# Kernel optimization log

Hardware: AMD Instinct MI355X
Metric: run time of the kernel (lower is better)

Reference implementation:

```python
import jax, jax.numpy as jnp
import numpy as np

BETA = 0.25
TEMP = 1.0
K = 1024          # codebook_size
DIM = 256         # dim == z_dim


def setup_inputs() -> dict:
    key = jax.random.key(0)
    k1, k2, k3 = jax.random.split(key, 3)
    x = jax.random.normal(k1, (8, 4096, DIM), dtype=jnp.float32)
    # Linear: kaiming_uniform -> sqrt(3/fan_in) * U(-1,1); bias init_bias=0 -> zeros
    W = np.sqrt(3.0 / DIM) * (jax.random.uniform(k2, (DIM, DIM), dtype=jnp.float32) * 2 - 1)
    b = jnp.zeros((DIM,), dtype=jnp.float32)
    # embedding: uniform(-1/K, 1/K)
    emb = jax.random.uniform(k3, (K, DIM), dtype=jnp.float32,
                             minval=-1.0 / K, maxval=1.0 / K)
    return {"x": x, "W": W, "b": b, "emb": emb}


def reference(x, W, b, emb):
    # proj_in: x @ W.T + b
    z = jnp.einsum('bld,od->blo', x, W) + b                     # [B, L, D]
    # squared-L2 distances to codebook (use_norm=False branch)
    dist = (jnp.sum(z * z, axis=-1, keepdims=True)
            + jnp.sum(emb * emb, axis=1)
            - 2.0 * jnp.einsum('bld,nd->bln', z, emb))           # [B, L, K]
    indices = jnp.argmin(dist, axis=-1)                          # [B, L] int
    # ste_prob computed in torch forward (affects grads via one_hot, not outputs)
    quant = emb[indices]                                         # [B, L, D]
    # commitment + codebook loss (training=True)
    loss = (BETA * jnp.mean((jax.lax.stop_gradient(quant) - z) ** 2)
            + jnp.mean((quant - jax.lax.stop_gradient(z)) ** 2))
    # straight-through estimator
    quant = z + jax.lax.stop_gradient(quant - z)
    return quant, indices, loss
```

## Files before the change

kernel.cpp:

```cpp
#include <hip/hip_runtime.h>
#include <hip/hip_bf16.h>

#define TT 32768
#define DD 256
#define KK 1024
#define B_S 5e-4f

typedef __attribute__((ext_vector_type(8)))  short bf16x8;
typedef __attribute__((ext_vector_type(4)))  short bf16x4s;
typedef __attribute__((ext_vector_type(16))) float f32x16;

static inline __device__ short f2bf(float v) {
    __hip_bfloat16 h = __float2bfloat16(v);
    return __builtin_bit_cast(short, h);
}
static inline __device__ float bf2f(short s) {
    __hip_bfloat16 h = __builtin_bit_cast(__hip_bfloat16, s);
    return __bfloat162float(h);
}

static inline __device__ void gload16(const void* g, void* l) {
    __builtin_amdgcn_global_load_lds(
        (const __attribute__((address_space(1))) void*)g,
        (__attribute__((address_space(3))) void*)l,
        16, 0, 0);
}

__global__ void k_ee(const float* __restrict__ emb, float* __restrict__ ee,
                     int* __restrict__ g_nf) {
    if (blockIdx.x == 0 && threadIdx.x == 0) g_nf[0] = 0;
    int n = blockIdx.x * 256 + threadIdx.x;
    if (n >= KK) return;
    const float4* r = (const float4*)(emb + (size_t)n * DD);
    float s = 0.f;
#pragma unroll
    for (int i = 0; i < DD / 4; ++i) {
        float4 v = r[i];
        s += v.x * v.x + v.y * v.y + v.z * v.z + v.w * v.w;
    }
    ee[n] = s;
}

__global__ void k_pack(const float* __restrict__ emb, short* __restrict__ pemb,
                       float4* __restrict__ embP4) {
    int u = blockIdx.x * 256 + threadIdx.x;
    int lane = u & 63;
    int ks  = (u >> 6) & 1, nb = (u >> 7) & 3;
    int kbi = (u >> 9) & 7, nc = (u >> 12) & 7;
    int n = nc * 128 + nb * 32 + (lane & 31);
    int k = kbi * 32 + ks * 16 + (lane >> 5) * 8;
    const float* src = emb + (size_t)n * DD + k;
    float4 v0 = *(const float4*)(src);
    float4 v1 = *(const float4*)(src + 4);
    bf16x8 hb = { f2bf(v0.x), f2bf(v0.y), f2bf(v0.z), f2bf(v0.w),
                  f2bf(v1.x), f2bf(v1.y), f2bf(v1.z), f2bf(v1.w) };
    *(bf16x8*)(pemb + (size_t)u * 8) = hb;
    embP4[(size_t)(k >> 2) * KK + n]       = v0;
    embP4[(size_t)((k >> 2) + 1) * KK + n] = v1;
}

#define PW 40

__launch_bounds__(256, 2)
__global__ void k_proj(const float* __restrict__ x, const float* __restrict__ W,
                       const float* __restrict__ bias, float* __restrict__ z) {
    __shared__ __align__(16) short Ax[3][64 * PW];
    __shared__ __align__(16) short Bw[3][256 * PW];
    const int tid = threadIdx.x;
    const int w = tid >> 6, lane = tid & 63;
    const int l31 = lane & 31, h = lane >> 5;
    const int t0 = blockIdx.x * 64;
    const int wt = (w & 1) * 32;
    const int wc = (w >> 1) * 128;

    f32x16 acc[4];
#pragma unroll
    for (int cb = 0; cb < 4; ++cb)
#pragma unroll
        for (int r = 0; r < 16; ++r) acc[cb][r] = 0.f;

    for (int kb = 0; kb < DD; kb += 32) {
        __syncthreads();
#pragma unroll
        for (int j = 0; j < 2; ++j) {
            int idx = j * 256 + tid, row = idx >> 3, c4 = idx & 7;
            float4 v = *(const float4*)(x + (size_t)(t0 + row) * DD + kb + c4 * 4);
            float e[4] = {v.x, v.y, v.z, v.w};
            bf16x4s s1, s2, s3;
#pragma unroll
            for (int q = 0; q < 4; ++q) {
                short h1 = f2bf(e[q]); float r1 = e[q] - bf2f(h1);
                short h2 = f2bf(r1);   float r2 = r1 - bf2f(h2);
                short h3 = f2bf(r2);
                s1[q] = h1; s2[q] = h2; s3[q] = h3;
            }
            int a = row * PW + c4 * 4;
            *(bf16x4s*)&Ax[0][a] = s1; *(bf16x4s*)&Ax[1][a] = s2; *(bf16x4s*)&Ax[2][a] = s3;
        }
#pragma unroll
        for (int j = 0; j < 8; ++j) {
            int idx = j * 256 + tid, row = idx >> 3, c4 = idx & 7;
            float4 v = *(const float4*)(W + (size_t)row * DD + kb + c4 * 4);
            float e[4] = {v.x, v.y, v.z, v.w};
            bf16x4s s1, s2, s3;
#pragma unroll
            for (int q = 0; q < 4; ++q) {
                short h1 = f2bf(e[q]); float r1 = e[q] - bf2f(h1);
                short h2 = f2bf(r1);   float r2 = r1 - bf2f(h2);
                short h3 = f2bf(r2);
                s1[q] = h1; s2[q] = h2; s3[q] = h3;
            }
            int a = row * PW + c4 * 4;
            *(bf16x4s*)&Bw[0][a] = s1; *(bf16x4s*)&Bw[1][a] = s2; *(bf16x4s*)&Bw[2][a] = s3;
        }
        __syncthreads();
#pragma unroll
        for (int ks = 0; ks < 2; ++ks) {
            int ao = (wt + l31) * PW + ks * 16 + h * 8;
            bf16x8 a1 = *(bf16x8*)&Ax[0][ao];
            bf16x8 a2 = *(bf16x8*)&Ax[1][ao];
            bf16x8 a3 = *(bf16x8*)&Ax[2][ao];
#pragma unroll
            for (int cb = 0; cb < 4; ++cb) {
                int bo = (wc + cb * 32 + l31) * PW + ks * 16 + h * 8;
                bf16x8 b1 = *(bf16x8*)&Bw[0][bo];
                bf16x8 b2 = *(bf16x8*)&Bw[1][bo];
                bf16x8 b3 = *(bf16x8*)&Bw[2][bo];
                acc[cb] = __builtin_amdgcn_mfma_f32_32x32x16_bf16(a1, b3, acc[cb], 0, 0, 0);
                acc[cb] = __builtin_amdgcn_mfma_f32_32x32x16_bf16(a2, b2, acc[cb], 0, 0, 0);
                acc[cb] = __builtin_amdgcn_mfma_f32_32x32x16_bf16(a3, b1, acc[cb], 0, 0, 0);
                acc[cb] = __builtin_amdgcn_mfma_f32_32x32x16_bf16(a1, b2, acc[cb], 0, 0, 0);
                acc[cb] = __builtin_amdgcn_mfma_f32_32x32x16_bf16(a2, b1, acc[cb], 0, 0, 0);
                acc[cb] = __builtin_amdgcn_mfma_f32_32x32x16_bf16(a1, b1, acc[cb], 0, 0, 0);
            }
        }
    }
#pragma unroll
    for (int cb = 0; cb < 4; ++cb) {
        int col = wc + cb * 32 + l31;
        float bc = bias[col];
#pragma unroll
        for (int r = 0; r < 16; ++r) {
            int row = (r & 3) + 8 * (r >> 2) + 4 * h;
            z[(size_t)(t0 + wt + row) * DD + col] = acc[cb][r] + bc;
        }
    }
}

#define SW 264

__launch_bounds__(256, 2)
__global__ void k_screen(const float* __restrict__ z, const short* __restrict__ pemb,
                         const float* __restrict__ ee_g, float* __restrict__ out_idx) {
    __shared__ __align__(16) char smem[65536];
    __shared__ float ee_s[1024];
    __shared__ float zzs[64];
    __shared__ float r_bv[64]; __shared__ int r_bi[64]; __shared__ float r_sv[64];

    short* A_s = (short*)smem;
    const int tid = threadIdx.x;
    const int w = tid >> 6, lane = tid & 63;
    const int l31 = lane & 31, h = lane >> 5;
    const int t0 = blockIdx.x * 64;
    const int wr = (w >> 1) * 32;
    const int hw = w & 1;

#pragma unroll
    for (int i = 0; i < 4; ++i) ee_s[i * 256 + tid] = ee_g[i * 256 + tid];

#pragma unroll
    for (int i = 0; i < 16; ++i) {
        int tl = i * 4 + w;
        float4 v = *(const float4*)(z + (size_t)(t0 + tl) * DD + lane * 4);
        float sq = v.x * v.x + v.y * v.y + v.z * v.z + v.w * v.w;
#pragma unroll
        for (int o = 32; o; o >>= 1) sq += __shfl_xor(sq, o);
        if (lane == 0) zzs[tl] = sq;
        bf16x4s hb = {f2bf(v.x), f2bf(v.y), f2bf(v.z), f2bf(v.w)};
        *(bf16x4s*)&A_s[tl * SW + lane * 4] = hb;
    }
    __syncthreads();

    bf16x8 af[16];
#pragma unroll
    for (int kbi = 0; kbi < 8; ++kbi)
#pragma unroll
        for (int ks = 0; ks < 2; ++ks)
            af[kbi * 2 + ks] = *(bf16x8*)&A_s[(wr + l31) * SW + kbi * 32 + ks * 16 + h * 8];
    __syncthreads();

    const char* pB = (const char*)pemb;
#pragma unroll
    for (int j = 0; j < 8; ++j)
        gload16(pB + j * 8192 + w * 1024 + lane * 16, smem + j * 4096 + w * 1024);

    float bestv[16], secv[16]; int besti[16];
#pragma unroll
    for (int r = 0; r < 16; ++r) { bestv[r] = 1e30f; secv[r] = 1e30f; besti[r] = 0; }

    for (int ph = 0; ph < 16; ++ph) {
        const int buf = ph & 1;
        char* Bb = smem + buf * 32768;
        asm volatile("s_waitcnt vmcnt(0)" ::: "memory");
        __syncthreads();
        if (ph < 15) {
            const int nn = ph + 1;
            const char* src = pB + (size_t)(nn >> 1) * 65536 + (nn & 1) * 4096;
            char* dst = smem + (buf ^ 1) * 32768;
#pragma unroll
            for (int j = 0; j < 8; ++j)
                gload16(src + j * 8192 + w * 1024 + lane * 16, dst + j * 4096 + w * 1024);
        }
        f32x16 acc;
#pragma unroll
        for (int r = 0; r < 16; ++r) acc[r] = 0.f;
#pragma unroll
        for (int kbi = 0; kbi < 8; ++kbi) {
            bf16x8 b0 = *(bf16x8*)(Bb + kbi * 4096 + (hw * 2 + 0) * 1024 + lane * 16);
            bf16x8 b1 = *(bf16x8*)(Bb + kbi * 4096 + (hw * 2 + 1) * 1024 + lane * 16);
            acc = __builtin_amdgcn_mfma_f32_32x32x16_bf16(af[kbi * 2 + 0], b0, acc, 0, 0, 0);
            acc = __builtin_amdgcn_mfma_f32_32x32x16_bf16(af[kbi * 2 + 1], b1, acc, 0, 0, 0);
        }
        {
            int n = (ph >> 1) * 128 + (ph & 1) * 64 + hw * 32 + l31;
            float en = ee_s[n];
#pragma unroll
            for (int r = 0; r < 16; ++r) {
                int row = (r & 3) + 8 * (r >> 2) + 4 * h;
                float u = zzs[wr + row] + en;
                float sc = fmaf(-2.f, acc[r], u);
                if (sc < bestv[r])      { secv[r] = bestv[r]; bestv[r] = sc; besti[r] = n; }
                else if (sc < secv[r])  { secv[r] = sc; }
            }
        }
    }

#pragma unroll
    for (int o = 1; o < 32; o <<= 1) {
#pragma unroll
        for (int r = 0; r < 16; ++r) {
            float ov = __shfl_xor(bestv[r], o);
            int   oi = __shfl_xor(besti[r], o);
            float os = __shfl_xor(secv[r], o);
            float mx = fmaxf(bestv[r], ov);
            secv[r] = fminf(fminf(secv[r], os), mx);
            if (ov < bestv[r] || (ov == bestv[r] && oi < besti[r])) { bestv[r] = ov; besti[r] = oi; }
        }
    }
    if ((w & 1) == 0 && l31 == 0) {
#pragma unroll
        for (int r = 0; r < 16; ++r) {
            int tr = wr + (r & 3) + 8 * (r >> 2) + 4 * h;
            r_bv[tr] = bestv[r]; r_bi[tr] = besti[r]; r_sv[tr] = secv[r];
        }
    }
    __syncthreads();
    if ((w & 1) == 1 && l31 == 0) {
#pragma unroll
        for (int r = 0; r < 16; ++r) {
            int tr = wr + (r & 3) + 8 * (r >> 2) + 4 * h;
            float lv = r_bv[tr]; int li = r_bi[tr]; float ls = r_sv[tr];
            float mx = fmaxf(lv, bestv[r]);
            float ns = fminf(fminf(ls, secv[r]), mx);
            float nv; int ni;
            if (bestv[r] < lv || (bestv[r] == lv && besti[r] < li)) { nv = bestv[r]; ni = besti[r]; }
            else { nv = lv; ni = li; }
            r_bv[tr] = nv; r_bi[tr] = ni; r_sv[tr] = ns;
        }
    }
    __syncthreads();
    if (tid < 64) {
        float bv = r_bv[tid], sv = r_sv[tid];
        int bi = r_bi[tid];
        float flag = ((sv - bv) < B_S) ? 4096.0f : 0.0f;
        out_idx[t0 + tid] = (float)bi + flag;
    }
}

__global__ void k_compact(const float* __restrict__ out_idx, int* __restrict__ g_nf,
                          int* __restrict__ g_list) {
    __shared__ int wbase[4];
    __shared__ int bbase;
    const int tid = threadIdx.x;
    const int t = blockIdx.x * 256 + tid;
    const int wid = tid >> 6, lane = tid & 63;
    bool fl = out_idx[t] >= 4096.0f;
    unsigned long long m = __ballot(fl);
    if (lane == 0) wbase[wid] = __popcll(m);
    __syncthreads();
    if (tid == 0) {
        int s = 0;
#pragma unroll
        for (int i = 0; i < 4; ++i) { int c = wbase[i]; wbase[i] = s; s += c; }
        bbase = atomicAdd(g_nf, s);
    }
    __syncthreads();
    if (fl) {
        int rank = __popcll(m & ((1ull << lane) - 1ull));
        g_list[bbase + wbase[wid] + rank] = t;
    }
}

#define RB 8

__launch_bounds__(256, 2)
__global__ void k_rescoreT(const float* __restrict__ z, const float4* __restrict__ embP4,
                           const float* __restrict__ ee_g, const int* __restrict__ g_nf,
                           const int* __restrict__ g_list, float* __restrict__ out_idx) {
    __shared__ float zrows[RB][256];
    __shared__ float zz8[RB];
    __shared__ int   toks[RB];
    __shared__ float rv_s[RB][4]; __shared__ int ri_s[RB][4];
    const int tid = threadIdx.x;
    const int w = tid >> 6, lane = tid & 63;
    const int nf = g_nf[0];

    for (int base = blockIdx.x * RB; base < nf; base += gridDim.x * RB) {
        __syncthreads();
        if (tid < RB) toks[tid] = (base + tid < nf) ? g_list[base + tid] : -1;
        __syncthreads();
#pragma unroll
        for (int qq = 0; qq < RB; ++qq) {
            int tok = toks[qq];
            zrows[qq][tid] = (tok >= 0) ? z[(size_t)tok * DD + tid] : 0.f;
        }
        __syncthreads();
        for (int qq = w; qq < RB; qq += 4) {
            float s = 0.f;
#pragma unroll
            for (int k = 0; k < 4; ++k) { float vv = zrows[qq][lane + 64 * k]; s += vv * vv; }
#pragma unroll
            for (int o = 32; o; o >>= 1) s += __shfl_xor(s, o);
            if (lane == 0) zz8[qq] = s;
        }
        __syncthreads();

        float en4[4];
#pragma unroll
        for (int p = 0; p < 4; ++p) en4[p] = ee_g[p * 256 + tid];

        float d[4][RB];
#pragma unroll
        for (int p = 0; p < 4; ++p)
#pragma unroll
            for (int q = 0; q < RB; ++q) d[p][q] = 0.f;

        float4 eA[4], eB[4], zA[RB], zB[RB];
#pragma unroll
        for (int p = 0; p < 4; ++p) eA[p] = embP4[(size_t)0 * KK + p * 256 + tid];
#pragma unroll
        for (int q = 0; q < RB; ++q) zA[q] = *(const float4*)&zrows[q][0];

        for (int k4 = 0; k4 < 64; k4 += 2) {
#pragma unroll
            for (int p = 0; p < 4; ++p) eB[p] = embP4[(size_t)(k4 + 1) * KK + p * 256 + tid];
#pragma unroll
            for (int q = 0; q < RB; ++q) zB[q] = *(const float4*)&zrows[q][(k4 + 1) * 4];
#pragma unroll
            for (int p = 0; p < 4; ++p)
#pragma unroll
                for (int q = 0; q < RB; ++q) {
                    d[p][q] = fmaf(eA[p].x, zA[q].x, d[p][q]);
                    d[p][q] = fmaf(eA[p].y, zA[q].y, d[p][q]);
                    d[p][q] = fmaf(eA[p].z, zA[q].z, d[p][q]);
                    d[p][q] = fmaf(eA[p].w, zA[q].w, d[p][q]);
                }
            if (k4 < 62) {
#pragma unroll
                for (int p = 0; p < 4; ++p) eA[p] = embP4[(size_t)(k4 + 2) * KK + p * 256 + tid];
#pragma unroll
                for (int q = 0; q < RB; ++q) zA[q] = *(const float4*)&zrows[q][(k4 + 2) * 4];
            }
#pragma unroll
            for (int p = 0; p < 4; ++p)
#pragma unroll
                for (int q = 0; q < RB; ++q) {
                    d[p][q] = fmaf(eB[p].x, zB[q].x, d[p][q]);
                    d[p][q] = fmaf(eB[p].y, zB[q].y, d[p][q]);
                    d[p][q] = fmaf(eB[p].z, zB[q].z, d[p][q]);
                    d[p][q] = fmaf(eB[p].w, zB[q].w, d[p][q]);
                }
        }

        float bv[RB]; int bi[RB];
#pragma unroll
        for (int q = 0; q < RB; ++q) { bv[q] = 1e30f; bi[q] = 0; }
#pragma unroll
        for (int p = 0; p < 4; ++p) {
            const int n = p * 256 + tid;
#pragma unroll
            for (int q = 0; q < RB; ++q) {
                float u = zz8[q] + en4[p];
                float s = fmaf(-2.f, d[p][q], u);
                if (s < bv[q]) { bv[q] = s; bi[q] = n; }
            }
        }
        for (int q = 0; q < RB; ++q) {
            float v = bv[q]; int i = bi[q];
#pragma unroll
            for (int o = 1; o < 64; o <<= 1) {
                float ov = __shfl_xor(v, o); int oi = __shfl_xor(i, o);
                if (ov < v || (ov == v && oi < i)) { v = ov; i = oi; }
            }
            if (lane == 0) { rv_s[q][w] = v; ri_s[q][w] = i; }
        }
        __syncthreads();
        if (tid < RB) {
            int tk = toks[tid];
            if (tk >= 0) {
                float fv = rv_s[tid][0]; int fi = ri_s[tid][0];
#pragma unroll
                for (int ww = 1; ww < 4; ++ww) {
                    if (rv_s[tid][ww] < fv || (rv_s[tid][ww] == fv && ri_s[tid][ww] < fi)) {
                        fv = rv_s[tid][ww]; fi = ri_s[tid][ww];
                    }
                }
                out_idx[tk] = (float)fi;
            }
        }
    }
}

__global__ void k_gather(float* __restrict__ zq, const float* __restrict__ emb,
                         const float* __restrict__ out_idx, float* __restrict__ partial) {
    __shared__ float red[4];
    const int tid = threadIdx.x;
    const int t0 = blockIdx.x * 128;
    const int tl = tid >> 1, part = tid & 1;
    int widx = (int)out_idx[t0 + tl];
    widx = min(max(widx, 0), KK - 1);
    const float* erow = emb + (size_t)widx * DD;
    float* qrow = zq + (size_t)(t0 + tl) * DD;
    float lsum = 0.f;
#pragma unroll
    for (int k = 0; k < 32; ++k) {
        int f = part + 2 * k;
        float4 e  = *(const float4*)(erow + f * 4);
        float4 zv = *(const float4*)(qrow + f * 4);
        float dx = e.x - zv.x, dy = e.y - zv.y, dz = e.z - zv.z, dw = e.w - zv.w;
        lsum += dx * dx + dy * dy + dz * dz + dw * dw;
        *(float4*)(qrow + f * 4) = e;
    }
#pragma unroll
    for (int off = 32; off; off >>= 1) lsum += __shfl_down(lsum, off);
    if ((tid & 63) == 0) red[tid >> 6] = lsum;
    __syncthreads();
    if (tid == 0) partial[blockIdx.x] = red[0] + red[1] + red[2] + red[3];
}

__global__ void k_loss(const float* __restrict__ partial, float* __restrict__ out_loss) {
    __shared__ float red[4];
    int tid = threadIdx.x;
    float s = partial[tid];
#pragma unroll
    for (int off = 32; off; off >>= 1) s += __shfl_down(s, off);
    if ((tid & 63) == 0) red[tid >> 6] = s;
    __syncthreads();
    if (tid == 0)
        out_loss[0] = (red[0] + red[1] + red[2] + red[3]) * (1.25f / 8388608.0f);
}

extern "C" void kernel_launch(void* const* d_in, const int* in_sizes, int n_in,
                              void* d_out, int out_size, void* d_ws, size_t ws_size,
                              hipStream_t stream) {
    const float* x   = (const float*)d_in[0];
    const float* W   = (const float*)d_in[1];
    const float* b   = (const float*)d_in[2];
    const float* emb = (const float*)d_in[3];

    float* out   = (float*)d_out;
    float* quant = out;
    float* oidx  = out + (size_t)TT * DD;
    float* oloss = oidx + TT;

    float* wsf     = (float*)d_ws;
    float* ee      = wsf;
    float* partial = wsf + 1024;
    short* pemb    = (short*)(wsf + 1280);
    int*   g_nf    = (int*)(wsf + 132352);
    int*   g_list  = (int*)(wsf + 132353);
    float4* embP4  = (float4*)(wsf + 165124);

    k_ee      <<<KK / 256, 256, 0, stream>>>(emb, ee, g_nf);
    k_pack    <<<128,      256, 0, stream>>>(emb, pemb, embP4);
    k_proj    <<<TT / 64,  256, 0, stream>>>(x, W, b, quant);
    k_screen  <<<TT / 64,  256, 0, stream>>>(quant, pemb, ee, oidx);
    k_compact <<<TT / 256, 256, 0, stream>>>(oidx, g_nf, g_list);
    k_rescoreT<<<512,      256, 0, stream>>>(quant, embP4, ee, g_nf, g_list, oidx);
    k_gather  <<<TT / 128, 256, 0, stream>>>(quant, emb, oidx, partial);
    k_loss    <<<1,        256, 0, stream>>>(partial, oloss);
}
```

Measured before the change: 275.0 us.

## Restructure screen kernel reductions via LDS and split MFMA accumulators

Replaces the shuffle-based row-norm and argmin/second-min reductions with LDS staging followed by serial per-row reductions in 64 threads. Splits the K-loop into two independent accumulator chains to shorten MFMA dependency latency, and hoists the per-row norms into registers. Launch bounds drop to one block per SM-slot hint, giving more registers. The tail now does a serial 64-entry loop per row, and the lower occupancy hint may reduce latency hiding.

```diff
diff --git a/kernel.cpp b/kernel.cpp
--- a/kernel.cpp
+++ b/kernel.cpp
@@ -149,15 +149,15 @@
 
 #define SW 264
 
-__launch_bounds__(256, 2)
+__launch_bounds__(256, 1)
 __global__ void k_screen(const float* __restrict__ z, const short* __restrict__ pemb,
                          const float* __restrict__ ee_g, float* __restrict__ out_idx) {
     __shared__ __align__(16) char smem[65536];
     __shared__ float ee_s[1024];
     __shared__ float zzs[64];
-    __shared__ float r_bv[64]; __shared__ int r_bi[64]; __shared__ float r_sv[64];
-
-    short* A_s = (short*)smem;
+
+    short* A_s   = (short*)smem;
+    float* zpart = (float*)(smem + 33792);
     const int tid = threadIdx.x;
     const int w = tid >> 6, lane = tid & 63;
     const int l31 = lane & 31, h = lane >> 5;
@@ -173,14 +173,27 @@
         int tl = i * 4 + w;
         float4 v = *(const float4*)(z + (size_t)(t0 + tl) * DD + lane * 4);
         float sq = v.x * v.x + v.y * v.y + v.z * v.z + v.w * v.w;
-#pragma unroll
-        for (int o = 32; o; o >>= 1) sq += __shfl_xor(sq, o);
-        if (lane == 0) zzs[tl] = sq;
+        zpart[tl * 65 + lane] = sq;
         bf16x4s hb = {f2bf(v.x), f2bf(v.y), f2bf(v.z), f2bf(v.w)};
         *(bf16x4s*)&A_s[tl * SW + lane * 4] = hb;
     }
     __syncthreads();
 
+    if (tid < 64) {
+        float t_[32];
+#pragma unroll
+        for (int l = 0; l < 32; ++l) t_[l] = zpart[tid * 65 + l] + zpart[tid * 65 + l + 32];
+#pragma unroll
+        for (int l = 0; l < 16; ++l) t_[l] = t_[l] + t_[l + 16];
+#pragma unroll
+        for (int l = 0; l < 8; ++l)  t_[l] = t_[l] + t_[l + 8];
+#pragma unroll
+        for (int l = 0; l < 4; ++l)  t_[l] = t_[l] + t_[l + 4];
+#pragma unroll
+        for (int l = 0; l < 2; ++l)  t_[l] = t_[l] + t_[l + 2];
+        zzs[tid] = t_[0] + t_[1];
+    }
+
     bf16x8 af[16];
 #pragma unroll
     for (int kbi = 0; kbi < 8; ++kbi)
@@ -188,6 +201,10 @@
         for (int ks = 0; ks < 2; ++ks)
             af[kbi * 2 + ks] = *(bf16x8*)&A_s[(wr + l31) * SW + kbi * 32 + ks * 16 + h * 8];
     __syncthreads();
+
+    float zf[16];
+#pragma unroll
+    for (int r = 0; r < 16; ++r) zf[r] = zzs[wr + (r & 3) + 8 * (r >> 2) + 4 * h];
 
     const char* pB = (const char*)pemb;
 #pragma unroll
@@ -211,67 +228,59 @@
             for (int j = 0; j < 8; ++j)
                 gload16(src + j * 8192 + w * 1024 + lane * 16, dst + j * 4096 + w * 1024);
         }
-        f32x16 acc;
-#pragma unroll
-        for (int r = 0; r < 16; ++r) acc[r] = 0.f;
-#pragma unroll
-        for (int kbi = 0; kbi < 8; ++kbi) {
-            bf16x8 b0 = *(bf16x8*)(Bb + kbi * 4096 + (hw * 2 + 0) * 1024 + lane * 16);
-            bf16x8 b1 = *(bf16x8*)(Bb + kbi * 4096 + (hw * 2 + 1) * 1024 + lane * 16);
-            acc = __builtin_amdgcn_mfma_f32_32x32x16_bf16(af[kbi * 2 + 0], b0, acc, 0, 0, 0);
-            acc = __builtin_amdgcn_mfma_f32_32x32x16_bf16(af[kbi * 2 + 1], b1, acc, 0, 0, 0);
+        f32x16 accA, accB;
+#pragma unroll
+        for (int r = 0; r < 16; ++r) { accA[r] = 0.f; accB[r] = 0.f; }
+#pragma unroll
+        for (int kbi = 0; kbi < 4; ++kbi) {
+            bf16x8 a0b = *(bf16x8*)(Bb + kbi * 4096 + (hw * 2 + 0) * 1024 + lane * 16);
+            bf16x8 a1b = *(bf16x8*)(Bb + kbi * 4096 + (hw * 2 + 1) * 1024 + lane * 16);
+            bf16x8 b0b = *(bf16x8*)(Bb + (kbi + 4) * 4096 + (hw * 2 + 0) * 1024 + lane * 16);
+            bf16x8 b1b = *(bf16x8*)(Bb + (kbi + 4) * 4096 + (hw * 2 + 1) * 1024 + lane * 16);
+            accA = __builtin_amdgcn_mfma_f32_32x32x16_bf16(af[kbi * 2 + 0], a0b, accA, 0, 0, 0);
+            accB = __builtin_amdgcn_mfma_f32_32x32x16_bf16(af[(kbi + 4) * 2 + 0], b0b, accB, 0, 0, 0);
+            accA = __builtin_amdgcn_mfma_f32_32x32x16_bf16(af[kbi * 2 + 1], a1b, accA, 0, 0, 0);
+            accB = __builtin_amdgcn_mfma_f32_32x32x16_bf16(af[(kbi + 4) * 2 + 1], b1b, accB, 0, 0, 0);
         }
         {
             int n = (ph >> 1) * 128 + (ph & 1) * 64 + hw * 32 + l31;
             float en = ee_s[n];
 #pragma unroll
             for (int r = 0; r < 16; ++r) {
-                int row = (r & 3) + 8 * (r >> 2) + 4 * h;
-                float u = zzs[wr + row] + en;
-                float sc = fmaf(-2.f, acc[r], u);
+                float u = zf[r] + en;
+                float d = accA[r] + accB[r];
+                float sc = fmaf(-2.f, d, u);
                 if (sc < bestv[r])      { secv[r] = bestv[r]; bestv[r] = sc; besti[r] = n; }
                 else if (sc < secv[r])  { secv[r] = sc; }
             }
         }
     }
 
-#pragma unroll
-    for (int o = 1; o < 32; o <<= 1) {
-#pragma unroll
-        for (int r = 0; r < 16; ++r) {
-            float ov = __shfl_xor(bestv[r], o);
-            int   oi = __shfl_xor(besti[r], o);
-            float os = __shfl_xor(secv[r], o);
-            float mx = fmaxf(bestv[r], ov);
-            secv[r] = fminf(fminf(secv[r], os), mx);
-            if (ov < bestv[r] || (ov == bestv[r] && oi < besti[r])) { bestv[r] = ov; besti[r] = oi; }
-        }
-    }
-    if ((w & 1) == 0 && l31 == 0) {
-#pragma unroll
-        for (int r = 0; r < 16; ++r) {
-            int tr = wr + (r & 3) + 8 * (r >> 2) + 4 * h;
-            r_bv[tr] = bestv[r]; r_bi[tr] = besti[r]; r_sv[tr] = secv[r];
-        }
-    }
-    __syncthreads();
-    if ((w & 1) == 1 && l31 == 0) {
-#pragma unroll
-        for (int r = 0; r < 16; ++r) {
-            int tr = wr + (r & 3) + 8 * (r >> 2) + 4 * h;
-            float lv = r_bv[tr]; int li = r_bi[tr]; float ls = r_sv[tr];
-            float mx = fmaxf(lv, bestv[r]);
-            float ns = fminf(fminf(ls, secv[r]), mx);
-            float nv; int ni;
-            if (bestv[r] < lv || (bestv[r] == lv && besti[r] < li)) { nv = bestv[r]; ni = besti[r]; }
-            else { nv = lv; ni = li; }
-            r_bv[tr] = nv; r_bi[tr] = ni; r_sv[tr] = ns;
-        }
+    __syncthreads();
+    float* entV = (float*)smem;
+    float* entS = entV + 4224;
+    int*   entI = (int*)(entV + 8448);
+    const int slot = hw * 32 + l31;
+#pragma unroll
+    for (int r = 0; r < 16; ++r) {
+        int tr = wr + (r & 3) + 8 * (r >> 2) + 4 * h;
+        entV[tr * 66 + slot] = bestv[r];
+        entS[tr * 66 + slot] = secv[r];
+        entI[tr * 66 + slot] = besti[r];
     }
     __syncthreads();
     if (tid < 64) {
-        float bv = r_bv[tid], sv = r_sv[tid];
-        int bi = r_bi[tid];
+        float bv = entV[tid * 66 + 0];
+        float sv = entS[tid * 66 + 0];
+        int   bi = entI[tid * 66 + 0];
+        for (int e = 1; e < 64; ++e) {
+            float v  = entV[tid * 66 + e];
+            float s2 = entS[tid * 66 + e];
+            int   i  = entI[tid * 66 + e];
+            float mx = fmaxf(bv, v);
+            sv = fminf(fminf(sv, s2), mx);
+            if (v < bv || (v == bv && i < bi)) { bv = v; bi = i; }
+        }
         float flag = ((sv - bv) < B_S) ? 4096.0f : 0.0f;
         out_idx[t0 + tid] = (float)bi + flag;
     }
```

New measurement: 259.6 us. 5.6% less time.

## Double screen tile to 128 tokens per 512-thread block, split MFMA chains, coalesce gather

Applied to the files above, without the earlier changes.

The screening kernel now processes 128 tokens per block with 8 waves, so each codebook tile staged in LDS is shared by twice as many rows and the per-wave load count halves. The MFMA K-loop is split into two independent accumulators to shorten the dependency chain, and row norms are hoisted into registers. The gather kernel is rewritten so each wave handles whole rows with coalesced float4 accesses. Risks include lower occupancy from the larger block and LDS footprint, and a slightly larger A staging area.

```diff
diff --git a/kernel.cpp b/kernel.cpp
--- a/kernel.cpp
+++ b/kernel.cpp
@@ -149,28 +149,28 @@
 
 #define SW 264
 
-__launch_bounds__(256, 2)
+__launch_bounds__(512, 2)
 __global__ void k_screen(const float* __restrict__ z, const short* __restrict__ pemb,
                          const float* __restrict__ ee_g, float* __restrict__ out_idx) {
-    __shared__ __align__(16) char smem[65536];
+    __shared__ __align__(16) char smem[67584];
     __shared__ float ee_s[1024];
-    __shared__ float zzs[64];
-    __shared__ float r_bv[64]; __shared__ int r_bi[64]; __shared__ float r_sv[64];
+    __shared__ float zzs[128];
+    __shared__ float r_bv[128]; __shared__ int r_bi[128]; __shared__ float r_sv[128];
 
     short* A_s = (short*)smem;
     const int tid = threadIdx.x;
     const int w = tid >> 6, lane = tid & 63;
     const int l31 = lane & 31, h = lane >> 5;
-    const int t0 = blockIdx.x * 64;
+    const int t0 = blockIdx.x * 128;
     const int wr = (w >> 1) * 32;
     const int hw = w & 1;
 
 #pragma unroll
-    for (int i = 0; i < 4; ++i) ee_s[i * 256 + tid] = ee_g[i * 256 + tid];
+    for (int i = 0; i < 2; ++i) ee_s[i * 512 + tid] = ee_g[i * 512 + tid];
 
 #pragma unroll
     for (int i = 0; i < 16; ++i) {
-        int tl = i * 4 + w;
+        int tl = i * 8 + w;
         float4 v = *(const float4*)(z + (size_t)(t0 + tl) * DD + lane * 4);
         float sq = v.x * v.x + v.y * v.y + v.z * v.z + v.w * v.w;
 #pragma unroll
@@ -189,10 +189,17 @@
             af[kbi * 2 + ks] = *(bf16x8*)&A_s[(wr + l31) * SW + kbi * 32 + ks * 16 + h * 8];
     __syncthreads();
 
+    float zf[16];
+#pragma unroll
+    for (int r = 0; r < 16; ++r) zf[r] = zzs[wr + (r & 3) + 8 * (r >> 2) + 4 * h];
+
     const char* pB = (const char*)pemb;
-#pragma unroll
-    for (int j = 0; j < 8; ++j)
-        gload16(pB + j * 8192 + w * 1024 + lane * 16, smem + j * 4096 + w * 1024);
+    const int pw4 = w >> 2, wb = (w & 3) * 1024;
+#pragma unroll
+    for (int j = 0; j < 4; ++j) {
+        int p = j * 2 + pw4;
+        gload16(pB + p * 8192 + wb + lane * 16, smem + p * 4096 + wb);
+    }
 
     float bestv[16], secv[16]; int besti[16];
 #pragma unroll
@@ -208,27 +215,33 @@
             const char* src = pB + (size_t)(nn >> 1) * 65536 + (nn & 1) * 4096;
             char* dst = smem + (buf ^ 1) * 32768;
 #pragma unroll
-            for (int j = 0; j < 8; ++j)
-                gload16(src + j * 8192 + w * 1024 + lane * 16, dst + j * 4096 + w * 1024);
-        }
-        f32x16 acc;
-#pragma unroll
-        for (int r = 0; r < 16; ++r) acc[r] = 0.f;
-#pragma unroll
-        for (int kbi = 0; kbi < 8; ++kbi) {
-            bf16x8 b0 = *(bf16x8*)(Bb + kbi * 4096 + (hw * 2 + 0) * 1024 + lane * 16);
-            bf16x8 b1 = *(bf16x8*)(Bb + kbi * 4096 + (hw * 2 + 1) * 1024 + lane * 16);
-            acc = __builtin_amdgcn_mfma_f32_32x32x16_bf16(af[kbi * 2 + 0], b0, acc, 0, 0, 0);
-            acc = __builtin_amdgcn_mfma_f32_32x32x16_bf16(af[kbi * 2 + 1], b1, acc, 0, 0, 0);
+            for (int j = 0; j < 4; ++j) {
+                int p = j * 2 + pw4;
+                gload16(src + p * 8192 + wb + lane * 16, dst + p * 4096 + wb);
+            }
+        }
+        f32x16 accA, accB;
+#pragma unroll
+        for (int r = 0; r < 16; ++r) { accA[r] = 0.f; accB[r] = 0.f; }
+#pragma unroll
+        for (int kbi = 0; kbi < 4; ++kbi) {
+            bf16x8 a0b = *(bf16x8*)(Bb + kbi * 4096 + (hw * 2 + 0) * 1024 + lane * 16);
+            bf16x8 a1b = *(bf16x8*)(Bb + kbi * 4096 + (hw * 2 + 1) * 1024 + lane * 16);
+            bf16x8 b0b = *(bf16x8*)(Bb + (kbi + 4) * 4096 + (hw * 2 + 0) * 1024 + lane * 16);
+            bf16x8 b1b = *(bf16x8*)(Bb + (kbi + 4) * 4096 + (hw * 2 + 1) * 1024 + lane * 16);
+            accA = __builtin_amdgcn_mfma_f32_32x32x16_bf16(af[kbi * 2 + 0], a0b, accA, 0, 0, 0);
+            accB = __builtin_amdgcn_mfma_f32_32x32x16_bf16(af[(kbi + 4) * 2 + 0], b0b, accB, 0, 0, 0);
+            accA = __builtin_amdgcn_mfma_f32_32x32x16_bf16(af[kbi * 2 + 1], a1b, accA, 0, 0, 0);
+            accB = __builtin_amdgcn_mfma_f32_32x32x16_bf16(af[(kbi + 4) * 2 + 1], b1b, accB, 0, 0, 0);
         }
         {
             int n = (ph >> 1) * 128 + (ph & 1) * 64 + hw * 32 + l31;
             float en = ee_s[n];
 #pragma unroll
             for (int r = 0; r < 16; ++r) {
-                int row = (r & 3) + 8 * (r >> 2) + 4 * h;
-                float u = zzs[wr + row] + en;
-                float sc = fmaf(-2.f, acc[r], u);
+                float u = zf[r] + en;
+                float d = accA[r] + accB[r];
+                float sc = fmaf(-2.f, d, u);
                 if (sc < bestv[r])      { secv[r] = bestv[r]; bestv[r] = sc; besti[r] = n; }
                 else if (sc < secv[r])  { secv[r] = sc; }
             }
@@ -247,6 +260,7 @@
             if (ov < bestv[r] || (ov == bestv[r] && oi < besti[r])) { bestv[r] = ov; besti[r] = oi; }
         }
     }
+    __syncthreads();
     if ((w & 1) == 0 && l31 == 0) {
 #pragma unroll
         for (int r = 0; r < 16; ++r) {
@@ -269,7 +283,7 @@
         }
     }
     __syncthreads();
-    if (tid < 64) {
+    if (tid < 128) {
         float bv = r_bv[tid], sv = r_sv[tid];
         int bi = r_bi[tid];
         float flag = ((sv - bv) < B_S) ? 4096.0f : 0.0f;
@@ -425,25 +439,23 @@
                          const float* __restrict__ out_idx, float* __restrict__ partial) {
     __shared__ float red[4];
     const int tid = threadIdx.x;
-    const int t0 = blockIdx.x * 128;
-    const int tl = tid >> 1, part = tid & 1;
-    int widx = (int)out_idx[t0 + tl];
-    widx = min(max(widx, 0), KK - 1);
-    const float* erow = emb + (size_t)widx * DD;
-    float* qrow = zq + (size_t)(t0 + tl) * DD;
+    const int w = tid >> 6, lane = tid & 63;
+    const int t0 = blockIdx.x * 128 + w * 32;
     float lsum = 0.f;
-#pragma unroll
-    for (int k = 0; k < 32; ++k) {
-        int f = part + 2 * k;
-        float4 e  = *(const float4*)(erow + f * 4);
-        float4 zv = *(const float4*)(qrow + f * 4);
+#pragma unroll 4
+    for (int i = 0; i < 32; ++i) {
+        const int t = t0 + i;
+        int widx = (int)out_idx[t];
+        widx = min(max(widx, 0), KK - 1);
+        float4 e  = *(const float4*)(emb + (size_t)widx * DD + lane * 4);
+        float4 zv = *(const float4*)(zq  + (size_t)t    * DD + lane * 4);
         float dx = e.x - zv.x, dy = e.y - zv.y, dz = e.z - zv.z, dw = e.w - zv.w;
         lsum += dx * dx + dy * dy + dz * dz + dw * dw;
-        *(float4*)(qrow + f * 4) = e;
+        *(float4*)(zq + (size_t)t * DD + lane * 4) = e;
     }
 #pragma unroll
     for (int off = 32; off; off >>= 1) lsum += __shfl_down(lsum, off);
-    if ((tid & 63) == 0) red[tid >> 6] = lsum;
+    if (lane == 0) red[w] = lsum;
     __syncthreads();
     if (tid == 0) partial[blockIdx.x] = red[0] + red[1] + red[2] + red[3];
 }
@@ -484,7 +496,7 @@
     k_ee      <<<KK / 256, 256, 0, stream>>>(emb, ee, g_nf);
     k_pack    <<<128,      256, 0, stream>>>(emb, pemb, embP4);
     k_proj    <<<TT / 64,  256, 0, stream>>>(x, W, b, quant);
-    k_screen  <<<TT / 64,  256, 0, stream>>>(quant, pemb, ee, oidx);
+    k_screen  <<<TT / 128, 512, 0, stream>>>(quant, pemb, ee, oidx);
     k_compact <<<TT / 256, 256, 0, stream>>>(oidx, g_nf, g_list);
     k_rescoreT<<<512,      256, 0, stream>>>(quant, embP4, ee, g_nf, g_list, oidx);
     k_gather  <<<TT / 128, 256, 0, stream>>>(quant, emb, oidx, partial);
```

Measured after the change: 271.6 us. No clear change (-1.2%).
